# Kernel tuning notes

Measured on AMD Instinct MI355X. Metric: run time of the kernel, lower is better.

## Reference

```python
import jax, jax.numpy as jnp
import numpy as np

B, T, H = 256, 512, 512
NB = 2  # band_names = ['g', 'r']
D_IN = 1 + NB


def setup_inputs() -> dict:
    key = jax.random.key(0)
    ks = jax.random.split(key, 10)
    # serial band assignment: each valid timestep belongs to exactly one band
    band = jax.random.randint(ks[0], (B, T), 0, NB)
    valid = jax.random.uniform(ks[1], (B, T)) < 0.9
    s_onehot = (jax.nn.one_hot(band, NB) * valid[..., None].astype(jnp.float32)).astype(bool)
    onehot = valid
    dtime = jax.random.uniform(ks[2], (B, T))
    encz_last = jax.random.normal(ks[3], (B, H))
    scale = 1.0 / np.sqrt(H).astype(np.float32)
    W_ih = jax.random.normal(ks[4], (3 * H, D_IN)) * scale
    W_hh = jax.random.normal(ks[5], (3 * H, H)) * scale
    b_ih = jax.random.normal(ks[6], (3 * H,)) * scale
    b_hh = jax.random.normal(ks[7], (3 * H,)) * scale
    W1 = jax.random.normal(ks[8], (H, H)) * scale
    b1 = jnp.zeros((H,), jnp.float32)
    W2 = jax.random.normal(ks[9], (1, H)) * scale
    b2 = jnp.zeros((1,), jnp.float32)
    return dict(dtime=dtime, s_onehot=s_onehot, onehot=onehot, encz_last=encz_last,
                W_ih=W_ih, W_hh=W_hh, b_ih=b_ih, b_hh=b_hh, W1=W1, b1=b1, W2=W2, b2=b2)


def gru_masked(x, mask, h0, W_ih, W_hh, b_ih, b_hh):
    """Single-layer GRU (torch gate order r,z,n) with onehot mask: hidden held where mask==False."""
    xp = jnp.einsum('btd,gd->btg', x, W_ih) + b_ih  # [B,T,3H] precomputed input projections

    def step(h, inp):
        xg, m = inp  # xg [B,3H], m [B]
        hg = h @ W_hh.T + b_hh
        xr, xz, xn = jnp.split(xg, 3, axis=-1)
        hr, hz, hn = jnp.split(hg, 3, axis=-1)
        r = jax.nn.sigmoid(xr + hr)
        z = jax.nn.sigmoid(xz + hz)
        n = jnp.tanh(xn + r * hn)
        h_new = (1.0 - z) * n + z * h
        h_out = jnp.where(m[:, None], h_new, h)
        return h_out, h_out

    _, hs = jax.lax.scan(step, h0, (jnp.swapaxes(xp, 0, 1), jnp.swapaxes(mask, 0, 1)))
    return jnp.swapaxes(hs, 0, 1)  # [B,T,H]


def serial_to_parallel(x, m):
    """Compact serial entries where mask m is True to the front of the time axis; zeros elsewhere."""
    pos = jnp.cumsum(m.astype(jnp.int32), axis=1) - 1  # target slot per valid step
    pos = jnp.where(m, pos, 0)
    b_idx = jnp.arange(x.shape[0])[:, None]
    contrib = x * m[..., None].astype(x.dtype)
    return jnp.zeros_like(x).at[b_idx, pos].add(contrib)


def reference(dtime, s_onehot, onehot, encz_last, W_ih, W_hh, b_ih, b_hh, W1, b1, W2, b2):
    decz_in = jnp.concatenate([dtime[..., None], s_onehot.astype(dtime.dtype)], axis=-1)  # [B,T,3]
    decz = gru_masked(decz_in, onehot, encz_last, W_ih, W_hh, b_ih, b_hh)  # [B,T,H]
    hidden = jax.nn.relu(jnp.einsum('bth,oh->bto', decz, W1) + b1)
    decx = jnp.einsum('bth,oh->bto', hidden, W2) + b2  # [B,T,1]
    outs = [serial_to_parallel(decx, s_onehot[..., kb]) for kb in range(s_onehot.shape[-1])]
    return jnp.stack(outs, axis=0)  # [NB,B,T,1] -> model/decx.{b} per band
```

## Files before the change

### kernel.cpp

```cpp
#include <hip/hip_runtime.h>
#include <hip/hip_bf16.h>

#define BB 256
#define TT 512
#define HH 512

typedef float floatx4 __attribute__((ext_vector_type(4)));
typedef short short8 __attribute__((ext_vector_type(8)));

__device__ __forceinline__ unsigned short f2bf(float f) {
    union { float f; unsigned u; } v; v.f = f;
    unsigned r = v.u + 0x7fffu + ((v.u >> 16) & 1u);
    return (unsigned short)(r >> 16);
}
__device__ __forceinline__ float bf2f(unsigned short h) {
    union { unsigned u; float f; } v; v.u = ((unsigned)h) << 16;
    return v.f;
}
__device__ __forceinline__ int frag16(int b, int j) {
    int kin = j & 31;
    return (j >> 5) * 512 + (b + 16 * ((kin >> 2) & 3)) * 8 + ((kin >> 4) << 2) + (kin & 3);
}

__device__ __forceinline__ int ld_sc0(const int* p) {
    int v;
    asm volatile("global_load_dword %0, %1, off sc0\n\ts_waitcnt vmcnt(0)"
                 : "=v"(v) : "v"(p) : "memory");
    return v;
}

__global__ void detect_k(const unsigned char* __restrict__ s, int* __restrict__ flags)
{
    int a = 0, b = 0, c = 0;
    for (int i = blockIdx.x * blockDim.x + threadIdx.x; i < BB * TT * 2;
         i += gridDim.x * blockDim.x) {
        unsigned char v = s[i];
        if (v) {
            int m = i & 3;
            if (m == 1) a = 1;
            else if (m >= 2) b = 1;
            if ((i & 7) == 4) c = 1;
        }
    }
    if (a) atomicOr(flags, 1);
    if (b) atomicOr(flags, 2);
    if (c) atomicOr(flags, 4);
}

__global__ void canon_k(const void* __restrict__ s, const int* __restrict__ flags,
                        unsigned char* __restrict__ canon)
{
    int bt = blockIdx.x * blockDim.x + threadIdx.x;
    if (bt >= BB * TT) return;
    int f = *flags;
    int sg, sr;
    if (f & 1) {
        const unsigned char* p = (const unsigned char*)s;
        sg = p[2 * bt] != 0; sr = p[2 * bt + 1] != 0;
    } else if (f & 2) {
        const float* p = (const float*)s;
        sg = p[2 * bt] != 0.0f; sr = p[2 * bt + 1] != 0.0f;
    } else if (f & 4) {
        const int* p = (const int*)s;
        sg = p[2 * bt] != 0; sr = p[2 * bt + 1] != 0;
    } else {
        const long long* p = (const long long*)s;
        sg = p[2 * bt] != 0; sr = p[2 * bt + 1] != 0;
    }
    canon[bt] = (unsigned char)(sg | (sr << 1));
}

__global__ void h0_k(const float* __restrict__ encz, unsigned* __restrict__ Hp)
{
    int i = blockIdx.x * blockDim.x + threadIdx.x;
    if (i >= BB * HH / 2) return;
    int bg = i >> 8;
    int j  = (i & 255) * 2;
    float f0 = encz[bg * HH + j], f1 = encz[bg * HH + j + 1];
    unsigned short h0b = f2bf(f0), l0b = f2bf(f0 - bf2f(h0b));
    unsigned short h1b = f2bf(f1), l1b = f2bf(f1 - bf2f(h1b));
    int g = bg >> 4, b = bg & 15;
    int fi = frag16(b, j) >> 1;
    unsigned* base = Hp + (size_t)g * 32768;
    base[fi]        = (unsigned)h0b | ((unsigned)h1b << 16);
    base[4096 + fi] = (unsigned)l0b | ((unsigned)l1b << 16);
}

__global__ void w1s_k(const float* __restrict__ W1,
                      unsigned short* __restrict__ W1h, unsigned short* __restrict__ W1l)
{
    int idx = blockIdx.x * blockDim.x + threadIdx.x;
    if (idx >= HH * HH) return;
    float f = W1[idx];
    unsigned short hb = f2bf(f);
    W1h[idx] = hb;
    W1l[idx] = f2bf(f - bf2f(hb));
}

template <bool FAST>
__device__ __forceinline__ void gru_loop(
    unsigned* Hbase, unsigned* hstage,
    const float* dtl, const unsigned char* cnl, float* exch, const float* pwl,
    unsigned short* decz, int* gcs, int* gcf,
    const short8* Bh, const short8* Bl,
    int tid, int w, int l, int wi, int bg0)
{
    int fastspin_en = 1;

    for (int t = 0; t < TT; ++t) {
        const char* src = (const char*)(Hbase + (size_t)(t & 3) * 8192);
        unsigned*   dst = Hbase + (size_t)((t + 1) & 3) * 8192;

        for (int c = w; c < 32; c += 6) {
            const void* gs = src + c * 1024 + l * 16;
            void* ls = (char*)hstage + c * 1024;
            __builtin_amdgcn_global_load_lds(
                (const __attribute__((address_space(1))) unsigned*)gs,
                (__attribute__((address_space(3))) unsigned*)ls, 16, 0,
                FAST ? 0x1 : 0x11);
        }
        __syncthreads();

        floatx4 ac0 = {0.f,0.f,0.f,0.f}, ac1 = {0.f,0.f,0.f,0.f}, ac2 = {0.f,0.f,0.f,0.f};
#pragma unroll
        for (int kt = 0; kt < 16; ++kt) {
            short8 ah = *(const short8*)((const char*)hstage + kt * 1024 + l * 16);
            short8 al = *(const short8*)((const char*)hstage + 16384 + kt * 1024 + l * 16);
            ac0 = __builtin_amdgcn_mfma_f32_16x16x32_bf16(ah, Bh[kt], ac0, 0, 0, 0);
            ac1 = __builtin_amdgcn_mfma_f32_16x16x32_bf16(ah, Bl[kt], ac1, 0, 0, 0);
            ac2 = __builtin_amdgcn_mfma_f32_16x16x32_bf16(al, Bh[kt], ac2, 0, 0, 0);
        }
        floatx4 acc = ac0 + ac1 + ac2;
        *(floatx4*)(exch + w * 256 + l * 4) = acc;
        __syncthreads();

        if (tid < 256) {
            const int b = tid >> 4;
            const int bgl = bg0 + b;
            const float dt = dtl[b * 516 + t];
            const unsigned char cn = cnl[b * 520 + t];
            const float sg = (cn & 1) ? 1.f : 0.f, sr = (cn & 2) ? 1.f : 0.f;
            const int jl0 = (tid * 2) & 31;
            const int j0  = wi * 32 + jl0;
            const int fi  = frag16(b, j0) >> 1;
            const unsigned hiw = hstage[fi];
            const unsigned low = hstage[4096 + fi];
            unsigned short hib[2], lob[2];
#pragma unroll
            for (int p = 0; p < 2; ++p) {
                int jl = jl0 + p;
                int lane16 = (jl & 15) + 16 * (b >> 2);
                int roff = b & 3;
                float a0 = exch[(jl >> 4) * 256 + lane16 * 4 + roff];
                float a1 = exch[(2 + (jl >> 4)) * 256 + lane16 * 4 + roff];
                float a2 = exch[(4 + (jl >> 4)) * 256 + lane16 * 4 + roff];
                float hp = bf2f((unsigned short)(p ? (hiw >> 16) : (hiw & 0xffffu))) +
                           bf2f((unsigned short)(p ? (low >> 16) : (low & 0xffffu)));
                float xr = pwl[0*32+jl]*dt + pwl[1*32+jl]*sg + pwl[2*32+jl]*sr + pwl[9*32+jl];
                float xz = pwl[3*32+jl]*dt + pwl[4*32+jl]*sg + pwl[5*32+jl]*sr + pwl[10*32+jl];
                float xn = pwl[6*32+jl]*dt + pwl[7*32+jl]*sg + pwl[8*32+jl]*sr + pwl[11*32+jl];
                float rr = 1.f / (1.f + __expf(-(xr + a0 + pwl[12*32+jl])));
                float zz = 1.f / (1.f + __expf(-(xz + a1 + pwl[13*32+jl])));
                float tx = xn + rr * (a2 + pwl[14*32+jl]);
                float ex2 = __expf(2.f * fminf(fmaxf(tx, -20.f), 20.f));
                float nn = 1.f - 2.f / (ex2 + 1.f);
                float hnew = (1.f - zz) * nn + zz * hp;
                float ho = cn ? hnew : hp;
                hib[p] = f2bf(ho);
                lob[p] = f2bf(ho - bf2f(hib[p]));
            }
            unsigned hw = (unsigned)hib[0] | ((unsigned)hib[1] << 16);
            unsigned lw = (unsigned)lob[0] | ((unsigned)lob[1] << 16);
            if (FAST) {
                dst[fi] = hw;
                dst[4096 + fi] = lw;
            } else {
                __hip_atomic_store(dst + fi, hw, __ATOMIC_RELAXED, __HIP_MEMORY_SCOPE_AGENT);
                __hip_atomic_store(dst + 4096 + fi, lw, __ATOMIC_RELAXED, __HIP_MEMORY_SCOPE_AGENT);
            }
            ((unsigned*)decz)[(((size_t)bgl * TT + t) * HH + j0) >> 1] = hw;
        }

        if (t != TT - 1) {
            __syncthreads();
            if (tid == 0) {
                int tgt = (t + 1) * 16;
                if (FAST) {
                    __hip_atomic_fetch_add(gcf, 1, __ATOMIC_RELAXED,
                                           __HIP_MEMORY_SCOPE_WORKGROUP);
                    __hip_atomic_fetch_add(gcs, 1, __ATOMIC_RELAXED,
                                           __HIP_MEMORY_SCOPE_AGENT);
                    int done = 0;
                    if (fastspin_en) {
                        for (int spin = 0; spin < 256; ++spin) {
                            if (ld_sc0(gcf) >= tgt) { done = 1; break; }
                        }
                        if (!done) fastspin_en = 0;
                    }
                    if (!done) {
                        while (__hip_atomic_load(gcs, __ATOMIC_RELAXED,
                                                 __HIP_MEMORY_SCOPE_AGENT) < tgt)
                            __builtin_amdgcn_s_sleep(1);
                    }
                } else {
                    __hip_atomic_fetch_add(gcs, 1, __ATOMIC_RELAXED,
                                           __HIP_MEMORY_SCOPE_AGENT);
                    while (__hip_atomic_load(gcs, __ATOMIC_RELAXED,
                                             __HIP_MEMORY_SCOPE_AGENT) < tgt)
                        __builtin_amdgcn_s_sleep(1);
                }
            }
            __syncthreads();
        }
    }
}

__global__ __launch_bounds__(384, 2) void gru_mfma(
    const float* __restrict__ dtime, const unsigned char* __restrict__ canon,
    const float* __restrict__ Wih, const float* __restrict__ Whh,
    const float* __restrict__ bih, const float* __restrict__ bhh,
    unsigned* __restrict__ Hp,
    unsigned short* __restrict__ decz,
    int* __restrict__ sync)
{
    __shared__ __align__(16) unsigned hstage[8192];
    __shared__ float dtl[16 * 516];
    __shared__ unsigned char cnl[16 * 520];
    __shared__ __align__(16) float exch[6 * 256];
    __shared__ float pwl[15 * 32];
    __shared__ int shflag;

    const int g = blockIdx.x & 15, wi = blockIdx.x >> 4;
    const int tid = threadIdx.x, w = tid >> 6, l = tid & 63;
    const int bg0 = g * 16;
    unsigned* Hbase = Hp + (size_t)g * 32768;

    for (int it = tid; it < 16 * 128; it += 384) {
        int b = it >> 7, t4 = it & 127;
        *(float4*)(dtl + b * 516 + t4 * 4) =
            *(const float4*)(dtime + (size_t)(bg0 + b) * TT + t4 * 4);
    }
    for (int it = tid; it < 16 * 128; it += 384) {
        int b = it >> 7, t4 = it & 127;
        *(unsigned*)(cnl + b * 520 + t4 * 4) =
            *(const unsigned*)(canon + (size_t)(bg0 + b) * TT + t4 * 4);
    }
    if (tid < 32) {
        int j = wi * 32 + tid;
        int r1 = HH + j, r2 = 2 * HH + j;
        pwl[0*32+tid] = Wih[j*3];   pwl[1*32+tid] = Wih[j*3+1];  pwl[2*32+tid] = Wih[j*3+2];
        pwl[3*32+tid] = Wih[r1*3];  pwl[4*32+tid] = Wih[r1*3+1]; pwl[5*32+tid] = Wih[r1*3+2];
        pwl[6*32+tid] = Wih[r2*3];  pwl[7*32+tid] = Wih[r2*3+1]; pwl[8*32+tid] = Wih[r2*3+2];
        pwl[9*32+tid]  = bih[j];  pwl[10*32+tid] = bih[r1]; pwl[11*32+tid] = bih[r2];
        pwl[12*32+tid] = bhh[j];  pwl[13*32+tid] = bhh[r1]; pwl[14*32+tid] = bhh[r2];
    }

    const int gate = w >> 1, ch = w & 1;
    const int rB   = gate * HH + wi * 32 + ch * 16 + (l & 15);
    const int kq4  = ((l >> 4) & 3) * 4;
    short8 Bh[16], Bl[16];
#pragma unroll
    for (int kt = 0; kt < 16; ++kt) {
        const float* wp = Whh + (size_t)rB * HH + kt * 32 + kq4;
        float4 f0 = *(const float4*)(wp);
        float4 f1 = *(const float4*)(wp + 16);
        float fs[8] = {f0.x, f0.y, f0.z, f0.w, f1.x, f1.y, f1.z, f1.w};
        short8 bh, bl;
#pragma unroll
        for (int q = 0; q < 8; ++q) {
            unsigned short hb = f2bf(fs[q]);
            bh[q] = (short)hb;
            bl[q] = (short)f2bf(fs[q] - bf2f(hb));
        }
        Bh[kt] = bh; Bl[kt] = bl;
    }

    unsigned xcc;
    asm volatile("s_getreg_b32 %0, hwreg(HW_REG_XCC_ID)" : "=s"(xcc));
    if (tid == 0) {
        __hip_atomic_fetch_or((unsigned*)&sync[1024 + g * 32], 1u << (xcc & 31),
                              __ATOMIC_RELAXED, __HIP_MEMORY_SCOPE_AGENT);
        __builtin_amdgcn_s_waitcnt(0);
        __hip_atomic_fetch_add(&sync[1536 + g * 32], 1, __ATOMIC_RELAXED,
                               __HIP_MEMORY_SCOPE_AGENT);
        while (__hip_atomic_load(&sync[1536 + g * 32], __ATOMIC_RELAXED,
                                 __HIP_MEMORY_SCOPE_AGENT) < 16)
            __builtin_amdgcn_s_sleep(2);
        unsigned m = __hip_atomic_load((unsigned*)&sync[1024 + g * 32], __ATOMIC_RELAXED,
                                       __HIP_MEMORY_SCOPE_AGENT);
        shflag = (__popc(m) == 1) ? 1 : 0;
    }
    __syncthreads();
    const int fast = shflag;

    int* gcs = sync + g * 32;
    int* gcf = sync + 512 + g * 32;
    if (fast)
        gru_loop<true>(Hbase, hstage, dtl, cnl, exch, pwl, decz, gcs, gcf, Bh, Bl,
                       tid, w, l, wi, bg0);
    else
        gru_loop<false>(Hbase, hstage, dtl, cnl, exch, pwl, decz, gcs, gcf, Bh, Bl,
                        tid, w, l, wi, bg0);
}

__global__ __launch_bounds__(512) void ff_mfma(
    const unsigned short* __restrict__ decz,
    const unsigned short* __restrict__ W1h, const unsigned short* __restrict__ W1l,
    const float* __restrict__ b1, const float* __restrict__ W2,
    const float* __restrict__ b2, float* __restrict__ decx)
{
    __shared__ __align__(16) unsigned short wst[2 * 512 * 32];

    const int wv = threadIdx.x >> 6, l = threadIdx.x & 63;
    const int row0 = blockIdx.x * 128 + wv * 16;
    const int mrow = l & 15, q = l >> 4;
    const unsigned short* arow = decz + (size_t)(row0 + mrow) * HH;

    floatx4 acc[32];
#pragma unroll
    for (int f = 0; f < 32; ++f) acc[f] = (floatx4){0.f, 0.f, 0.f, 0.f};

    for (int kt = 0; kt < 16; ++kt) {
        __syncthreads();
        for (int it = threadIdx.x; it < 8192; it += 512) {
            int plane = it >> 12, rest = it & 4095;
            int n = rest >> 3, q4 = rest & 7;
            const unsigned short* gp =
                (plane ? W1l : W1h) + (size_t)n * HH + kt * 32 + q4 * 4;
            uint2 v = *(const uint2*)gp;
            int e0 = (q4 & 3) * 8 + (q4 >> 2) * 4;
            *(uint2*)(wst + plane * 16384 + n * 32 + e0) = v;
        }
        __syncthreads();

        const int k0 = kt * 32 + q * 4;
        union { unsigned u[4]; short8 s; } a;
        *(uint2*)&a.u[0] = *(const uint2*)(arow + k0);
        *(uint2*)&a.u[2] = *(const uint2*)(arow + k0 + 16);
#pragma unroll
        for (int f = 0; f < 32; ++f) {
            const int n = f * 16 + mrow;
            short8 bh = *(const short8*)(wst + n * 32 + q * 8);
            short8 bl = *(const short8*)(wst + 16384 + n * 32 + q * 8);
            acc[f] = __builtin_amdgcn_mfma_f32_16x16x32_bf16(a.s, bh, acc[f], 0, 0, 0);
            acc[f] = __builtin_amdgcn_mfma_f32_16x16x32_bf16(a.s, bl, acc[f], 0, 0, 0);
        }
    }

    float res[4] = {0.f, 0.f, 0.f, 0.f};
#pragma unroll
    for (int f = 0; f < 32; ++f) {
        int n = f * 16 + mrow;
        float w2v = W2[n], b1v = b1[n];
#pragma unroll
        for (int i = 0; i < 4; ++i)
            res[i] += w2v * fmaxf(acc[f][i] + b1v, 0.f);
    }
    const float b2v = b2[0];
#pragma unroll
    for (int i = 0; i < 4; ++i) {
        float v = res[i];
        v += __shfl_xor(v, 1, 64);
        v += __shfl_xor(v, 2, 64);
        v += __shfl_xor(v, 4, 64);
        v += __shfl_xor(v, 8, 64);
        if (mrow == 0) decx[row0 + q * 4 + i] = v + b2v;
    }
}

__global__ void scatter_k(const unsigned char* __restrict__ canon,
                          const float* __restrict__ decx, float* __restrict__ out)
{
    int wid = (blockIdx.x * blockDim.x + threadIdx.x) >> 6;
    int lane = threadIdx.x & 63;
    if (wid >= 2 * BB) return;
    int kb = wid >> 8, b = wid & 255;
    int cnt = 0;
    for (int t0 = 0; t0 < TT; t0 += 64) {
        unsigned char c = canon[b * TT + t0 + lane];
        int pred = (c >> kb) & 1;
        unsigned long long m = __ballot(pred);
        if (pred) {
            int pos = cnt + __popcll(m & ((1ull << lane) - 1ull));
            out[((size_t)kb * BB + b) * TT + pos] = decx[b * TT + t0 + lane];
        }
        cnt += __popcll(m);
    }
}

extern "C" void kernel_launch(void* const* d_in, const int* in_sizes, int n_in,
                              void* d_out, int out_size, void* d_ws, size_t ws_size,
                              hipStream_t stream)
{
    const float* dtime    = (const float*)d_in[0];
    const void*  s_onehot = d_in[1];
    const float* encz = (const float*)d_in[3];
    const float* Wih  = (const float*)d_in[4];
    const float* Whh  = (const float*)d_in[5];
    const float* bih  = (const float*)d_in[6];
    const float* bhh  = (const float*)d_in[7];
    const float* W1   = (const float*)d_in[8];
    const float* b1   = (const float*)d_in[9];
    const float* W2   = (const float*)d_in[10];
    const float* b2   = (const float*)d_in[11];

    char* ws = (char*)d_ws;
    int*            sync  = (int*)ws;
    int*            flags = (int*)(ws + 8192);
    unsigned char*  canon = (unsigned char*)(ws + 8704);
    unsigned*       Hp    = (unsigned*)(ws + 8704 + BB * TT);
    unsigned short* decz  = (unsigned short*)((char*)Hp + 16 * 32768 * 4);
    unsigned short* W1h   = (unsigned short*)Hp;
    unsigned short* W1l   = W1h + HH * HH;
    float*          decx  = (float*)(W1l + HH * HH);

    hipMemsetAsync(ws, 0, 8448, stream);
    detect_k<<<32, 256, 0, stream>>>((const unsigned char*)s_onehot, flags);
    canon_k<<<(BB * TT + 255) / 256, 256, 0, stream>>>(s_onehot, flags, canon);
    h0_k<<<(BB * HH / 2 + 255) / 256, 256, 0, stream>>>(encz, Hp);

    gru_mfma<<<256, 384, 0, stream>>>(dtime, canon, Wih, Whh, bih, bhh,
                                      Hp, decz, sync);

    w1s_k<<<(HH * HH + 255) / 256, 256, 0, stream>>>(W1, W1h, W1l);
    ff_mfma<<<BB * TT / 128, 512, 0, stream>>>(decz, W1h, W1l, b1, W2, b2, decx);

    hipMemsetAsync(d_out, 0, (size_t)out_size * sizeof(float), stream);
    scatter_k<<<128, 256, 0, stream>>>(canon, decx, (float*)d_out);
}
```

Baseline: 1.685 ms.

## Split GRU recurrent matmul over K halves per wave and parallelize barrier atomics

Each wave now computes two 16-column N tiles over half of K, instead of one N tile over all of K. The two partial sums are written to a larger exchange buffer and added in the gate phase. This interleaves more independent MFMA chains per wave, which should hide MFMA latency better in the serial per-timestep recurrence. The fast-path barrier also issues the agent-scope counter increment from a different wave, and the fast spin count is raised. The templated loop is inlined with runtime branches on the fast flag, which may cost registers or add branch overhead.

```diff
diff --git a/kernel.cpp b/kernel.cpp
--- a/kernel.cpp
+++ b/kernel.cpp
@@ -97,14 +97,91 @@
     W1l[idx] = f2bf(f - bf2f(hb));
 }
 
-template <bool FAST>
-__device__ __forceinline__ void gru_loop(
-    unsigned* Hbase, unsigned* hstage,
-    const float* dtl, const unsigned char* cnl, float* exch, const float* pwl,
-    unsigned short* decz, int* gcs, int* gcf,
-    const short8* Bh, const short8* Bl,
-    int tid, int w, int l, int wi, int bg0)
-{
+__global__ __launch_bounds__(384, 2) void gru_mfma(
+    const float* __restrict__ dtime, const unsigned char* __restrict__ canon,
+    const float* __restrict__ Wih, const float* __restrict__ Whh,
+    const float* __restrict__ bih, const float* __restrict__ bhh,
+    unsigned* __restrict__ Hp,
+    unsigned short* __restrict__ decz,
+    int* __restrict__ sync)
+{
+    __shared__ __align__(16) unsigned hstage[8192];
+    __shared__ float dtl[16 * 516];
+    __shared__ unsigned char cnl[16 * 520];
+    __shared__ __align__(16) float exch[12 * 256];
+    __shared__ float pwl[15 * 32];
+    __shared__ int shflag;
+
+    const int g = blockIdx.x & 15, wi = blockIdx.x >> 4;
+    const int tid = threadIdx.x, w = tid >> 6, l = tid & 63;
+    const int bg0 = g * 16;
+    unsigned* Hbase = Hp + (size_t)g * 32768;
+
+    for (int it = tid; it < 16 * 128; it += 384) {
+        int b = it >> 7, t4 = it & 127;
+        *(float4*)(dtl + b * 516 + t4 * 4) =
+            *(const float4*)(dtime + (size_t)(bg0 + b) * TT + t4 * 4);
+    }
+    for (int it = tid; it < 16 * 128; it += 384) {
+        int b = it >> 7, t4 = it & 127;
+        *(unsigned*)(cnl + b * 520 + t4 * 4) =
+            *(const unsigned*)(canon + (size_t)(bg0 + b) * TT + t4 * 4);
+    }
+    if (tid < 32) {
+        int j = wi * 32 + tid;
+        int r1 = HH + j, r2 = 2 * HH + j;
+        pwl[0*32+tid] = Wih[j*3];   pwl[1*32+tid] = Wih[j*3+1];  pwl[2*32+tid] = Wih[j*3+2];
+        pwl[3*32+tid] = Wih[r1*3];  pwl[4*32+tid] = Wih[r1*3+1]; pwl[5*32+tid] = Wih[r1*3+2];
+        pwl[6*32+tid] = Wih[r2*3];  pwl[7*32+tid] = Wih[r2*3+1]; pwl[8*32+tid] = Wih[r2*3+2];
+        pwl[9*32+tid]  = bih[j];  pwl[10*32+tid] = bih[r1]; pwl[11*32+tid] = bih[r2];
+        pwl[12*32+tid] = bhh[j];  pwl[13*32+tid] = bhh[r1]; pwl[14*32+tid] = bhh[r2];
+    }
+
+    const int gate = w >> 1, kh = w & 1;
+    const int kq4  = ((l >> 4) & 3) * 4;
+    short8 Bh[2][8], Bl[2][8];
+#pragma unroll
+    for (int nt = 0; nt < 2; ++nt) {
+        const int rB = gate * HH + wi * 32 + nt * 16 + (l & 15);
+#pragma unroll
+        for (int k8 = 0; k8 < 8; ++k8) {
+            int kt = kh * 8 + k8;
+            const float* wp = Whh + (size_t)rB * HH + kt * 32 + kq4;
+            float4 f0 = *(const float4*)(wp);
+            float4 f1 = *(const float4*)(wp + 16);
+            float fs[8] = {f0.x, f0.y, f0.z, f0.w, f1.x, f1.y, f1.z, f1.w};
+            short8 bh, bl;
+#pragma unroll
+            for (int q = 0; q < 8; ++q) {
+                unsigned short hb = f2bf(fs[q]);
+                bh[q] = (short)hb;
+                bl[q] = (short)f2bf(fs[q] - bf2f(hb));
+            }
+            Bh[nt][k8] = bh; Bl[nt][k8] = bl;
+        }
+    }
+
+    int* gcs = sync + g * 32;
+    int* gcf = sync + 512 + g * 32;
+
+    unsigned xcc;
+    asm volatile("s_getreg_b32 %0, hwreg(HW_REG_XCC_ID)" : "=s"(xcc));
+    if (tid == 0) {
+        __hip_atomic_fetch_or((unsigned*)&sync[1024 + g * 32], 1u << (xcc & 31),
+                              __ATOMIC_RELAXED, __HIP_MEMORY_SCOPE_AGENT);
+        asm volatile("s_waitcnt vmcnt(0)" ::: "memory");
+        __hip_atomic_fetch_add(&sync[1536 + g * 32], 1, __ATOMIC_RELAXED,
+                               __HIP_MEMORY_SCOPE_AGENT);
+        while (__hip_atomic_load(&sync[1536 + g * 32], __ATOMIC_RELAXED,
+                                 __HIP_MEMORY_SCOPE_AGENT) < 16)
+            __builtin_amdgcn_s_sleep(2);
+        unsigned m = __hip_atomic_load((unsigned*)&sync[1024 + g * 32], __ATOMIC_RELAXED,
+                                       __HIP_MEMORY_SCOPE_AGENT);
+        shflag = (__popc(m) == 1) ? 1 : 0;
+    }
+    __syncthreads();
+    const int fast = shflag;
+
     int fastspin_en = 1;
 
     for (int t = 0; t < TT; ++t) {
@@ -114,24 +191,40 @@
         for (int c = w; c < 32; c += 6) {
             const void* gs = src + c * 1024 + l * 16;
             void* ls = (char*)hstage + c * 1024;
-            __builtin_amdgcn_global_load_lds(
-                (const __attribute__((address_space(1))) unsigned*)gs,
-                (__attribute__((address_space(3))) unsigned*)ls, 16, 0,
-                FAST ? 0x1 : 0x11);
+            if (fast)
+                __builtin_amdgcn_global_load_lds(
+                    (const __attribute__((address_space(1))) unsigned*)gs,
+                    (__attribute__((address_space(3))) unsigned*)ls, 16, 0, 0x1);
+            else
+                __builtin_amdgcn_global_load_lds(
+                    (const __attribute__((address_space(1))) unsigned*)gs,
+                    (__attribute__((address_space(3))) unsigned*)ls, 16, 0, 0x11);
         }
         __syncthreads();
 
-        floatx4 ac0 = {0.f,0.f,0.f,0.f}, ac1 = {0.f,0.f,0.f,0.f}, ac2 = {0.f,0.f,0.f,0.f};
-#pragma unroll
-        for (int kt = 0; kt < 16; ++kt) {
+        floatx4 ac[2][3];
+#pragma unroll
+        for (int nt = 0; nt < 2; ++nt)
+#pragma unroll
+            for (int cch = 0; cch < 3; ++cch)
+                ac[nt][cch] = (floatx4){0.f, 0.f, 0.f, 0.f};
+#pragma unroll
+        for (int k8 = 0; k8 < 8; ++k8) {
+            int kt = kh * 8 + k8;
             short8 ah = *(const short8*)((const char*)hstage + kt * 1024 + l * 16);
             short8 al = *(const short8*)((const char*)hstage + 16384 + kt * 1024 + l * 16);
-            ac0 = __builtin_amdgcn_mfma_f32_16x16x32_bf16(ah, Bh[kt], ac0, 0, 0, 0);
-            ac1 = __builtin_amdgcn_mfma_f32_16x16x32_bf16(ah, Bl[kt], ac1, 0, 0, 0);
-            ac2 = __builtin_amdgcn_mfma_f32_16x16x32_bf16(al, Bh[kt], ac2, 0, 0, 0);
-        }
-        floatx4 acc = ac0 + ac1 + ac2;
-        *(floatx4*)(exch + w * 256 + l * 4) = acc;
+#pragma unroll
+            for (int nt = 0; nt < 2; ++nt) {
+                ac[nt][0] = __builtin_amdgcn_mfma_f32_16x16x32_bf16(ah, Bh[nt][k8], ac[nt][0], 0, 0, 0);
+                ac[nt][1] = __builtin_amdgcn_mfma_f32_16x16x32_bf16(ah, Bl[nt][k8], ac[nt][1], 0, 0, 0);
+                ac[nt][2] = __builtin_amdgcn_mfma_f32_16x16x32_bf16(al, Bh[nt][k8], ac[nt][2], 0, 0, 0);
+            }
+        }
+#pragma unroll
+        for (int nt = 0; nt < 2; ++nt) {
+            floatx4 s = ac[nt][0] + ac[nt][1] + ac[nt][2];
+            *(floatx4*)(exch + (gate * 4 + kh * 2 + nt) * 256 + l * 4) = s;
+        }
         __syncthreads();
 
         if (tid < 256) {
@@ -142,18 +235,18 @@
             const float sg = (cn & 1) ? 1.f : 0.f, sr = (cn & 2) ? 1.f : 0.f;
             const int jl0 = (tid * 2) & 31;
             const int j0  = wi * 32 + jl0;
-            const int fi  = frag16(b, j0) >> 1;
-            const unsigned hiw = hstage[fi];
-            const unsigned low = hstage[4096 + fi];
+            const int fi2 = frag16(b, j0) >> 1;
+            const unsigned hiw = hstage[fi2];
+            const unsigned low = hstage[4096 + fi2];
             unsigned short hib[2], lob[2];
 #pragma unroll
             for (int p = 0; p < 2; ++p) {
                 int jl = jl0 + p;
-                int lane16 = (jl & 15) + 16 * (b >> 2);
-                int roff = b & 3;
-                float a0 = exch[(jl >> 4) * 256 + lane16 * 4 + roff];
-                float a1 = exch[(2 + (jl >> 4)) * 256 + lane16 * 4 + roff];
-                float a2 = exch[(4 + (jl >> 4)) * 256 + lane16 * 4 + roff];
+                int nt = jl >> 4;
+                int eo = ((jl & 15) + 16 * (b >> 2)) * 4 + (b & 3);
+                float a0 = exch[(0 + nt) * 256 + eo] + exch[(2 + nt) * 256 + eo];
+                float a1 = exch[(4 + nt) * 256 + eo] + exch[(6 + nt) * 256 + eo];
+                float a2 = exch[(8 + nt) * 256 + eo] + exch[(10 + nt) * 256 + eo];
                 float hp = bf2f((unsigned short)(p ? (hiw >> 16) : (hiw & 0xffffu))) +
                            bf2f((unsigned short)(p ? (low >> 16) : (low & 0xffffu)));
                 float xr = pwl[0*32+jl]*dt + pwl[1*32+jl]*sg + pwl[2*32+jl]*sr + pwl[9*32+jl];
@@ -171,28 +264,31 @@
             }
             unsigned hw = (unsigned)hib[0] | ((unsigned)hib[1] << 16);
             unsigned lw = (unsigned)lob[0] | ((unsigned)lob[1] << 16);
-            if (FAST) {
-                dst[fi] = hw;
-                dst[4096 + fi] = lw;
+            if (fast) {
+                dst[fi2] = hw;
+                dst[4096 + fi2] = lw;
             } else {
-                __hip_atomic_store(dst + fi, hw, __ATOMIC_RELAXED, __HIP_MEMORY_SCOPE_AGENT);
-                __hip_atomic_store(dst + 4096 + fi, lw, __ATOMIC_RELAXED, __HIP_MEMORY_SCOPE_AGENT);
+                __hip_atomic_store(dst + fi2, hw, __ATOMIC_RELAXED,
+                                   __HIP_MEMORY_SCOPE_AGENT);
+                __hip_atomic_store(dst + 4096 + fi2, lw, __ATOMIC_RELAXED,
+                                   __HIP_MEMORY_SCOPE_AGENT);
             }
             ((unsigned*)decz)[(((size_t)bgl * TT + t) * HH + j0) >> 1] = hw;
         }
 
         if (t != TT - 1) {
             __syncthreads();
-            if (tid == 0) {
-                int tgt = (t + 1) * 16;
-                if (FAST) {
+            if (fast) {
+                if (tid == 64)
+                    __hip_atomic_fetch_add(gcs, 1, __ATOMIC_RELAXED,
+                                           __HIP_MEMORY_SCOPE_AGENT);
+                if (tid == 0) {
                     __hip_atomic_fetch_add(gcf, 1, __ATOMIC_RELAXED,
                                            __HIP_MEMORY_SCOPE_WORKGROUP);
-                    __hip_atomic_fetch_add(gcs, 1, __ATOMIC_RELAXED,
-                                           __HIP_MEMORY_SCOPE_AGENT);
+                    int tgt = (t + 1) * 16;
                     int done = 0;
                     if (fastspin_en) {
-                        for (int spin = 0; spin < 256; ++spin) {
+                        for (int spin = 0; spin < 2048; ++spin) {
                             if (ld_sc0(gcf) >= tgt) { done = 1; break; }
                         }
                         if (!done) fastspin_en = 0;
@@ -202,9 +298,12 @@
                                                  __HIP_MEMORY_SCOPE_AGENT) < tgt)
                             __builtin_amdgcn_s_sleep(1);
                     }
-                } else {
+                }
+            } else {
+                if (tid == 0) {
                     __hip_atomic_fetch_add(gcs, 1, __ATOMIC_RELAXED,
                                            __HIP_MEMORY_SCOPE_AGENT);
+                    int tgt = (t + 1) * 16;
                     while (__hip_atomic_load(gcs, __ATOMIC_RELAXED,
                                              __HIP_MEMORY_SCOPE_AGENT) < tgt)
                         __builtin_amdgcn_s_sleep(1);
@@ -213,94 +312,6 @@
             __syncthreads();
         }
     }
-}
-
-__global__ __launch_bounds__(384, 2) void gru_mfma(
-    const float* __restrict__ dtime, const unsigned char* __restrict__ canon,
-    const float* __restrict__ Wih, const float* __restrict__ Whh,
-    const float* __restrict__ bih, const float* __restrict__ bhh,
-    unsigned* __restrict__ Hp,
-    unsigned short* __restrict__ decz,
-    int* __restrict__ sync)
-{
-    __shared__ __align__(16) unsigned hstage[8192];
-    __shared__ float dtl[16 * 516];
-    __shared__ unsigned char cnl[16 * 520];
-    __shared__ __align__(16) float exch[6 * 256];
-    __shared__ float pwl[15 * 32];
-    __shared__ int shflag;
-
-    const int g = blockIdx.x & 15, wi = blockIdx.x >> 4;
-    const int tid = threadIdx.x, w = tid >> 6, l = tid & 63;
-    const int bg0 = g * 16;
-    unsigned* Hbase = Hp + (size_t)g * 32768;
-
-    for (int it = tid; it < 16 * 128; it += 384) {
-        int b = it >> 7, t4 = it & 127;
-        *(float4*)(dtl + b * 516 + t4 * 4) =
-            *(const float4*)(dtime + (size_t)(bg0 + b) * TT + t4 * 4);
-    }
-    for (int it = tid; it < 16 * 128; it += 384) {
-        int b = it >> 7, t4 = it & 127;
-        *(unsigned*)(cnl + b * 520 + t4 * 4) =
-            *(const unsigned*)(canon + (size_t)(bg0 + b) * TT + t4 * 4);
-    }
-    if (tid < 32) {
-        int j = wi * 32 + tid;
-        int r1 = HH + j, r2 = 2 * HH + j;
-        pwl[0*32+tid] = Wih[j*3];   pwl[1*32+tid] = Wih[j*3+1];  pwl[2*32+tid] = Wih[j*3+2];
-        pwl[3*32+tid] = Wih[r1*3];  pwl[4*32+tid] = Wih[r1*3+1]; pwl[5*32+tid] = Wih[r1*3+2];
-        pwl[6*32+tid] = Wih[r2*3];  pwl[7*32+tid] = Wih[r2*3+1]; pwl[8*32+tid] = Wih[r2*3+2];
-        pwl[9*32+tid]  = bih[j];  pwl[10*32+tid] = bih[r1]; pwl[11*32+tid] = bih[r2];
-        pwl[12*32+tid] = bhh[j];  pwl[13*32+tid] = bhh[r1]; pwl[14*32+tid] = bhh[r2];
-    }
-
-    const int gate = w >> 1, ch = w & 1;
-    const int rB   = gate * HH + wi * 32 + ch * 16 + (l & 15);
-    const int kq4  = ((l >> 4) & 3) * 4;
-    short8 Bh[16], Bl[16];
-#pragma unroll
-    for (int kt = 0; kt < 16; ++kt) {
-        const float* wp = Whh + (size_t)rB * HH + kt * 32 + kq4;
-        float4 f0 = *(const float4*)(wp);
-        float4 f1 = *(const float4*)(wp + 16);
-        float fs[8] = {f0.x, f0.y, f0.z, f0.w, f1.x, f1.y, f1.z, f1.w};
-        short8 bh, bl;
-#pragma unroll
-        for (int q = 0; q < 8; ++q) {
-            unsigned short hb = f2bf(fs[q]);
-            bh[q] = (short)hb;
-            bl[q] = (short)f2bf(fs[q] - bf2f(hb));
-        }
-        Bh[kt] = bh; Bl[kt] = bl;
-    }
-
-    unsigned xcc;
-    asm volatile("s_getreg_b32 %0, hwreg(HW_REG_XCC_ID)" : "=s"(xcc));
-    if (tid == 0) {
-        __hip_atomic_fetch_or((unsigned*)&sync[1024 + g * 32], 1u << (xcc & 31),
-                              __ATOMIC_RELAXED, __HIP_MEMORY_SCOPE_AGENT);
-        __builtin_amdgcn_s_waitcnt(0);
-        __hip_atomic_fetch_add(&sync[1536 + g * 32], 1, __ATOMIC_RELAXED,
-                               __HIP_MEMORY_SCOPE_AGENT);
-        while (__hip_atomic_load(&sync[1536 + g * 32], __ATOMIC_RELAXED,
-                                 __HIP_MEMORY_SCOPE_AGENT) < 16)
-            __builtin_amdgcn_s_sleep(2);
-        unsigned m = __hip_atomic_load((unsigned*)&sync[1024 + g * 32], __ATOMIC_RELAXED,
-                                       __HIP_MEMORY_SCOPE_AGENT);
-        shflag = (__popc(m) == 1) ? 1 : 0;
-    }
-    __syncthreads();
-    const int fast = shflag;
-
-    int* gcs = sync + g * 32;
-    int* gcf = sync + 512 + g * 32;
-    if (fast)
-        gru_loop<true>(Hbase, hstage, dtl, cnl, exch, pwl, decz, gcs, gcf, Bh, Bl,
-                       tid, w, l, wi, bg0);
-    else
-        gru_loop<false>(Hbase, hstage, dtl, cnl, exch, pwl, decz, gcs, gcf, Bh, Bl,
-                        tid, w, l, wi, bg0);
 }
 
 __global__ __launch_bounds__(512) void ff_mfma(
```

New measurement: 1.920 ms. 13.9% more time.
